# Performance work log

Measured on AMD Instinct MI355X. Metric: run time of the kernel, lower is better.

The kernel has to match this reference:

```python
import jax, jax.numpy as jnp
import numpy as np

B, L, D, H = 32, 128, 300, 1024
VOCAB = 32000


def setup_inputs() -> dict:
    key = jax.random.key(0)
    ks = jax.random.split(key, 8)
    sentence_embedding = jax.random.normal(ks[0], (B, L, D), dtype=jnp.float32)
    sentence_word = jax.random.randint(ks[1], (B, L), 0, VOCAB, dtype=jnp.int32)
    length = jax.random.randint(ks[2], (B,), L // 2, L + 1, dtype=jnp.int32)
    # leaf LSTMCell params (torch layout: weight [4H, in], gate order i,f,g,o)
    W_ih = jax.random.normal(ks[3], (4 * H, D), dtype=jnp.float32) * (2.0 / D) ** 0.5
    W_hh = jax.random.normal(ks[4], (4 * H, H), dtype=jnp.float32) * (1.0 / H) ** 0.5
    b_ih = jnp.zeros((4 * H,), jnp.float32).at[H:2 * H].set(1.0)  # forget bias = 1
    b_hh = jnp.zeros((4 * H,), jnp.float32)
    # NaryLSTMLayer: cat[h_l, h_x, h_r] (3H) -> gates i, f_l, f_x, f_r, u, o (6H)
    W_comp = jax.random.normal(ks[5], (6 * H, 3 * H), dtype=jnp.float32) * (2.0 / (3 * H)) ** 0.5
    b_comp = jnp.zeros((6 * H,), jnp.float32)
    return dict(sentence_embedding=sentence_embedding, W_ih=W_ih, W_hh=W_hh,
                b_ih=b_ih, b_hh=b_hh, W_comp=W_comp, b_comp=b_comp,
                sentence_word=sentence_word, length=length)


def _leaf_lstm(x, W_ih, W_hh, b_ih, b_hh):
    # x: (B, L, D) -> hs, cs: (B, L, H); vectorized over batch, scan over time
    h = W_hh.shape[1]
    h0 = jnp.zeros((x.shape[0], h), x.dtype)

    def step(carry, x_t):
        hp, cp = carry
        gates = x_t @ W_ih.T + b_ih + hp @ W_hh.T + b_hh
        i, f, g, o = jnp.split(gates, 4, axis=-1)
        c = jax.nn.sigmoid(f) * cp + jax.nn.sigmoid(i) * jnp.tanh(g)
        hn = jax.nn.sigmoid(o) * jnp.tanh(c)
        return (hn, c), (hn, c)

    _, (hs, cs) = jax.lax.scan(step, (h0, h0), jnp.swapaxes(x, 0, 1))
    return jnp.swapaxes(hs, 0, 1), jnp.swapaxes(cs, 0, 1)


def _compose(l, r, x, W_comp, b_comp):
    hl, cl = l
    hr, cr = r
    hx, cx = x
    a = jnp.concatenate([hl, hx, hr], axis=-1) @ W_comp.T + b_comp
    i, fl, fx, fr, u, o = jnp.split(a, 6, axis=-1)
    c = (jax.nn.sigmoid(i) * jnp.tanh(u) + jax.nn.sigmoid(fl) * cl
         + jax.nn.sigmoid(fx) * cx + jax.nn.sigmoid(fr) * cr)
    return jax.nn.sigmoid(o) * jnp.tanh(c), c


def _greedy_build(hs_i, cs_i, sc, start, end, zero, W_comp, b_comp):
    # sc: concrete numpy scores -> tree structure is a trace-time constant
    if end == start:
        return None
    if end == start + 1:
        return (hs_i[start], cs_i[start])
    pos = start + int(np.argmax(sc[start:end]))
    l = _greedy_build(hs_i, cs_i, sc, start, pos, zero, W_comp, b_comp)
    r = _greedy_build(hs_i, cs_i, sc, pos + 1, end, zero, W_comp, b_comp)
    if l is None:
        l = (zero, zero)
    if r is None:
        r = (zero, zero)
    return _compose(l, r, (hs_i[pos], cs_i[pos]), W_comp, b_comp)


def reference(sentence_embedding, W_ih, W_hh, b_ih, b_hh, W_comp, b_comp,
              sentence_word, length):
    hdim = W_hh.shape[1]
    hs, cs = _leaf_lstm(sentence_embedding, W_ih, W_hh, b_ih, b_hh)
    words = np.asarray(sentence_word)
    lens = np.asarray(length)
    # calc_score: 1 / (1 + df); vocab.id_to_df emulated as (w % 1000) + 1
    scores = 1.0 / (2.0 + (words % 1000).astype(np.float64))
    zero = jnp.zeros((hdim,), sentence_embedding.dtype)
    h_res, c_res = [], []
    for b in range(words.shape[0]):
        state = _greedy_build(hs[b], cs[b], scores[b], 0, int(lens[b]), zero,
                              W_comp, b_comp)
        h_res.append(state[0])
        c_res.append(state[1])
    return jnp.stack(h_res, axis=0), jnp.stack(c_res, axis=0)
```

## Files before the change

### kernel.cpp

```cpp
#include <hip/hip_runtime.h>

typedef unsigned short u16;
typedef __attribute__((ext_vector_type(8))) short short8;
typedef __attribute__((ext_vector_type(4))) float floatx4;

#define B_   32
#define L_   128
#define D_   300
#define DP_  320
#define H_   1024
#define G4_  4096
#define K3_  3072
#define NROUNDS 40

#define MO_MAXLEV 0
#define MO_ROOT   8
#define MO_LSTART 64
#define MO_LCOUNT 256
#define MO_FLG    448
#define MO_NODES  512
#define MO_CNT    4608
#define SPIN_CAP  500000
#define SPIN_CAP2 200000

#define FGRID 256
#define FTHREADS 512

#define MFMA(a,b,c) __builtin_amdgcn_mfma_f32_16x16x32_bf16((a),(b),(c),0,0,0)

__device__ inline float b2f(u16 u){ union { unsigned int i; float f; } v; v.i = ((unsigned int)u) << 16; return v.f; }
__device__ inline u16 f2b(float f){ union { float f; unsigned int i; } v; v.f = f; unsigned int r = v.i + 0x7FFFu + ((v.i >> 16) & 1u); return (u16)(r >> 16); }
__device__ inline float h2f(u16 u){ union { _Float16 h; u16 s; } v; v.s = u; return (float)v.h; }
__device__ inline u16 f2h(float f){ union { _Float16 h; u16 s; } v; v.h = (_Float16)f; return v.s; }
__device__ inline float sigf(float x){ return 1.f / (1.f + __expf(-x)); }
__device__ inline float tanh_(float x){ return 1.f - 2.f / (__expf(2.f * x) + 1.f); }
__device__ inline short8 cvt8(const float* p){
  floatx4 a = *(const floatx4*)p, b = *(const floatx4*)(p + 4);
  short8 r;
  r[0]=(short)f2b(a[0]); r[1]=(short)f2b(a[1]); r[2]=(short)f2b(a[2]); r[3]=(short)f2b(a[3]);
  r[4]=(short)f2b(b[0]); r[5]=(short)f2b(b[1]); r[6]=(short)f2b(b[2]); r[7]=(short)f2b(b[3]);
  return r;
}

__global__ void k_init(const float* __restrict__ emb, const float* __restrict__ Wih,
                       const float* __restrict__ Wcomp,
                       u16* __restrict__ embP, u16* __restrict__ WihP,
                       u16* __restrict__ WcompB,
                       u16* __restrict__ nodeH, float* __restrict__ nodeC, int* meta)
{
  const int gtid = blockIdx.x * 256 + threadIdx.x;
  const int nT = 2048 * 256;
  if (gtid < 64) meta[MO_FLG + gtid] = 0;
  for (int i = gtid; i < B_ * H_; i += nT) {
    int b = i >> 10, c = i & (H_ - 1);
    nodeH[(size_t)(b * 129 + 128) * H_ + c] = 0;
    nodeC[(size_t)(b * 129 + 128) * H_ + c] = 0.f;
  }
  for (int i = gtid; i < B_ * L_ * DP_; i += nT) {
    int r = i / DP_, k = i - r * DP_;
    embP[i] = (k < D_) ? f2b(emb[(size_t)r * D_ + k]) : (u16)0;
  }
  for (int i = gtid; i < G4_ * DP_; i += nT) {
    int r = i / DP_, k = i - r * DP_;
    WihP[i] = (k < D_) ? f2b(Wih[(size_t)r * D_ + k]) : (u16)0;
  }
  if (WcompB) {
    for (int c = gtid; c < (6 * H_ * K3_) / 8; c += nT)
      *(short8*)(WcompB + (size_t)c * 8) = cvt8(Wcomp + (size_t)c * 8);
  }
}

__global__ __launch_bounds__(256) void k_xg(const u16* __restrict__ embP,
    const u16* __restrict__ WihP, const float* __restrict__ bih,
    const float* __restrict__ bhh, u16* __restrict__ Xg)
{
  const int lane = threadIdx.x & 63, wave = threadIdx.x >> 6;
  const int l15 = lane & 15, quad = lane >> 4;
  const int gw = blockIdx.x * 4 + wave;
  for (int st = gw; st < 128 * 128; st += 2048 * 4) {
    int tm = st >> 7, tn = st & 127;
    int m0 = tm * 32, n0 = tn * 32;
    floatx4 acc[2][2] = {};
    for (int kc = 0; kc < DP_ / 32; ++kc) {
      int ko = kc * 32 + quad * 8;
      short8 a0 = *(const short8*)(embP + (size_t)(m0 + l15) * DP_ + ko);
      short8 a1 = *(const short8*)(embP + (size_t)(m0 + 16 + l15) * DP_ + ko);
      short8 b0 = *(const short8*)(WihP + (size_t)(n0 + l15) * DP_ + ko);
      short8 b1 = *(const short8*)(WihP + (size_t)(n0 + 16 + l15) * DP_ + ko);
      acc[0][0] = MFMA(a0, b0, acc[0][0]);
      acc[0][1] = MFMA(a0, b1, acc[0][1]);
      acc[1][0] = MFMA(a1, b0, acc[1][0]);
      acc[1][1] = MFMA(a1, b1, acc[1][1]);
    }
    for (int mi = 0; mi < 2; ++mi)
      for (int ni = 0; ni < 2; ++ni)
        for (int r = 0; r < 4; ++r) {
          int m = m0 + mi * 16 + quad * 4 + r;
          int n = n0 + ni * 16 + l15;
          float v = acc[mi][ni][r] + bih[n] + bhh[n];
          Xg[(size_t)m * G4_ + n] = f2h(v);
        }
  }
}

#define SCAN_LDS (65536 + 4*32*17*4)
__global__ __launch_bounds__(256, 1) void k_scan(const float* __restrict__ Whh,
    const u16* __restrict__ Xg, u16* __restrict__ nodeH,
    float* __restrict__ nodeC, u16* __restrict__ hEx, int* meta)
{
  extern __shared__ char smem[];
  u16*   hst = (u16*)smem;
  float* sG  = (float*)(smem + 65536);
  const int tid = threadIdx.x;
  const int g = tid >> 6, lane = tid & 63;
  const int l15 = lane & 15, quad = lane >> 4;
  const int n16 = blockIdx.x;
  int* flags = meta + MO_FLG;

  short8 bf[32];
#pragma unroll
  for (int kc = 0; kc < 32; ++kc)
    bf[kc] = cvt8(Whh + ((size_t)(g * 1024 + n16 * 16 + l15)) * 1024 + kc * 32 + quad * 8);

  const int cb = g * 8 + (lane & 7);
  const int cp = lane >> 3;
  const int c0 = n16 * 16 + cp * 2;

  float cst0 = 0.f, cst1 = 0.f;
  for (int t = 0; t < L_; ++t) {
    float xv[4][2];
    {
      const u16* xr = Xg + (size_t)(cb * 128 + t) * G4_;
#pragma unroll
      for (int gg = 0; gg < 4; ++gg)
#pragma unroll
        for (int u = 0; u < 2; ++u)
          xv[gg][u] = h2f(xr[gg * 1024 + c0 + u]);
    }
    floatx4 acc[2] = {};
    if (t > 0) {
      const unsigned long long* src =
          (const unsigned long long*)(hEx + ((t - 1) & 1) * (B_ * H_));
#pragma unroll
      for (int ch = 0; ch < 2; ++ch) {
        unsigned long long tmp[16];
#pragma unroll
        for (int q = 0; q < 16; ++q)
          tmp[q] = __hip_atomic_load(src + (ch * 16 + q) * 256 + tid,
                                     __ATOMIC_RELAXED, __HIP_MEMORY_SCOPE_AGENT);
#pragma unroll
        for (int q = 0; q < 16; ++q) {
          int idx = (ch * 16 + q) * 256 + tid;
          int b = idx >> 8, g8 = idx & 255, gr = g8 >> 1;
          *(unsigned long long*)(hst + (b << 10) + ((gr ^ (b & 7)) << 3) + (g8 & 1) * 4) = tmp[q];
        }
      }
      __syncthreads();
#pragma unroll
      for (int kc = 0; kc < 32; ++kc) {
        int gr = (kc * 4 + quad) ^ (l15 & 7);
        short8 a0 = *(const short8*)(hst + (l15 << 10) + (gr << 3));
        short8 a1 = *(const short8*)(hst + ((16 + l15) << 10) + (gr << 3));
        acc[0] = MFMA(a0, bf[kc], acc[0]);
        acc[1] = MFMA(a1, bf[kc], acc[1]);
      }
    }
#pragma unroll
    for (int mt = 0; mt < 2; ++mt)
#pragma unroll
      for (int r = 0; r < 4; ++r)
        sG[(g * 32 + mt * 16 + quad * 4 + r) * 17 + l15] = acc[mt][r];
    __syncthreads();
    {
      float cc[2] = { cst0, cst1 };
      float hh[2];
#pragma unroll
      for (int u = 0; u < 2; ++u) {
        int col = cp * 2 + u;
        float iv = sG[(0 * 32 + cb) * 17 + col] + xv[0][u];
        float fv = sG[(1 * 32 + cb) * 17 + col] + xv[1][u];
        float gv = sG[(2 * 32 + cb) * 17 + col] + xv[2][u];
        float ov = sG[(3 * 32 + cb) * 17 + col] + xv[3][u];
        float c = sigf(fv) * cc[u] + sigf(iv) * tanh_(gv);
        float h = sigf(ov) * tanh_(c);
        cc[u] = c; hh[u] = h;
      }
      cst0 = cc[0]; cst1 = cc[1];
      unsigned pack = (unsigned)f2b(hh[0]) | ((unsigned)f2b(hh[1]) << 16);
      __hip_atomic_store((unsigned*)(hEx + (t & 1) * (B_ * H_)) + (cb << 9) + (c0 >> 1),
                         pack, __ATOMIC_RELAXED, __HIP_MEMORY_SCOPE_AGENT);
      *(unsigned*)(nodeH + (size_t)(cb * 129 + t) * H_ + c0) = pack;
      *(float2*)(nodeC + (size_t)(cb * 129 + t) * H_ + c0) = make_float2(cc[0], cc[1]);
    }
    __syncthreads();
    if (tid == 0)
      __hip_atomic_store(&flags[n16], t + 1, __ATOMIC_RELAXED, __HIP_MEMORY_SCOPE_AGENT);
    if (g == 0) {
      int it = 0;
      for (;;) {
        int v = __hip_atomic_load(&flags[lane], __ATOMIC_RELAXED, __HIP_MEMORY_SCOPE_AGENT);
        if (__all(v >= t + 1) || ++it >= SPIN_CAP) break;
        __builtin_amdgcn_s_sleep(1);
      }
    }
    __syncthreads();
  }
}

__global__ void k_tree(const int* __restrict__ words, const int* __restrict__ lens,
                       int* meta)
{
  const int tid = threadIdx.x;
  __shared__ u16 sD[B_][L_];
  __shared__ short sL[B_][L_], sR[B_][L_];
  __shared__ short sS[B_][130];
  __shared__ short sO[B_][L_];
  __shared__ unsigned char sLev[B_][L_];
  __shared__ int sHist[132], sCur[132], sMaxLev;
  for (int i = tid; i < 132; i += 256) { sHist[i] = 0; sCur[i] = 0; }
  if (tid == 0) sMaxLev = 1;
  for (int i = tid; i < 256; i += 256) meta[MO_CNT + i] = 0;
  for (int i = tid; i < B_ * L_; i += 256) {
    int b = i >> 7, t = i & 127;
    sD[b][t] = (u16)(words[i] % 1000);
    sL[b][t] = -1; sR[b][t] = -1; sLev[b][t] = 0;
  }
  __syncthreads();
  if (tid < B_) {
    const int b = tid;
    int len = lens[b];
    if (len < 2) len = 2;
    if (len > 128) len = 128;
    int sp = 0;
    for (int i = 0; i < len; ++i) {
      int v = sD[b][i];
      int last = -1;
      while (sp > 0) {
        int top = sS[b][sp - 1];
        if ((int)sD[b][top] > v) { last = top; --sp; } else break;
      }
      sL[b][i] = (short)last;
      if (sp > 0) sR[b][sS[b][sp - 1]] = (short)i;
      sS[b][sp++] = (short)i;
    }
    const int root = sS[b][0];
    meta[MO_ROOT + b] = root;
    int cnt = 0, tp = 0;
    sS[b][tp++] = (short)root;
    while (tp > 0) {
      int p = sS[b][--tp];
      sO[b][cnt++] = (short)p;
      int l = sL[b][p], r = sR[b][p];
      if (l >= 0) sS[b][tp++] = (short)l;
      if (r >= 0) sS[b][tp++] = (short)r;
    }
    for (int k = cnt - 1; k >= 0; --k) {
      int p = sO[b][k];
      int l = sL[b][p], r = sR[b][p];
      if (l >= 0 || r >= 0) {
        int hl = (l >= 0) ? (int)sLev[b][l] : 0;
        int hr = (r >= 0) ? (int)sLev[b][r] : 0;
        sLev[b][p] = (unsigned char)(1 + (hl > hr ? hl : hr));
      }
    }
    atomicMax(&sMaxLev, (int)sLev[b][root]);
    for (int p = 0; p < len; ++p)
      if (sLev[b][p]) atomicAdd(&sHist[sLev[b][p]], 1);
  }
  __syncthreads();
  if (tid == 0) {
    int off2 = 0;
    for (int r = 1; r <= 128; ++r) {
      meta[MO_LSTART + r] = off2;
      sCur[r] = off2;
      meta[MO_LCOUNT + r] = sHist[r];
      off2 += sHist[r];
    }
    meta[MO_MAXLEV] = sMaxLev;
  }
  __syncthreads();
  if (tid < B_) {
    const int b = tid;
    int len = lens[b];
    if (len < 2) len = 2;
    if (len > 128) len = 128;
    for (int p = 0; p < len; ++p) if (sLev[b][p]) {
      int l = sL[b][p], r = sR[b][p];
      int le = (l < 0) ? 128 : (sLev[b][l] ? 129 + l : l);
      int re = (r < 0) ? 128 : (sLev[b][r] ? 129 + r : r);
      int idx = atomicAdd(&sCur[sLev[b][p]], 1);
      meta[MO_NODES + idx] = (b << 25) | (p << 18) | (le << 9) | re;
    }
  }
}

#define FOREST_LDS (147456 + 12288 + 512)
__global__ __launch_bounds__(FTHREADS, 2) void k_forest(const u16* __restrict__ Wc,
    const float* __restrict__ bcomp, const u16* __restrict__ nodeH,
    const float* __restrict__ nodeC, u16* __restrict__ compH,
    float* __restrict__ compC, int* meta)
{
  extern __shared__ char smem[];
  u16*   wlds  = (u16*)smem;
  float* sG    = (float*)(smem + 147456);
  int*   sInfo = (int*)(smem + 147456 + 12288);
  const int bcol = blockIdx.x;
  const int tid = threadIdx.x;
  const int w = tid >> 6, lane = tid & 63;
  const int l15 = lane & 15, quad = lane >> 4;
  int* flg = meta + MO_CNT;
  const int maxLev = meta[MO_MAXLEV];

  for (int j = tid; j < 9216; j += FTHREADS) {
    int idx = j / 24, r24 = j - idx * 24;
    int G = (r24 >> 2) * 1024 + bcol * 4 + (r24 & 3);
    *(short8*)(wlds + (size_t)j * 8) = *(const short8*)(Wc + (size_t)G * K3_ + idx * 8);
  }
  __syncthreads();

  for (int rd = 1; rd <= maxLev && rd <= 128; ++rd) {
    const int M = meta[MO_LCOUNT + rd];
    const int base = meta[MO_LSTART + rd];
    const int ntiles = (M + 127) >> 7;
    for (int tile = 0; tile < ntiles; ++tile) {
      __syncthreads();
      if (tid < 128) {
        int j = tile * 128 + tid; if (j >= M) j = M - 1;
        sInfo[tid] = meta[MO_NODES + base + j];
      }
      __syncthreads();
      {
        int info = sInfo[w * 16 + l15];
        int b = (info >> 25) & 31, p = (info >> 18) & 127;
        int li = (info >> 9) & 0x1FF, ri = info & 0x1FF;
        const u16* A0 = (li <= 128) ? nodeH + ((size_t)(b * 129 + li) << 10)
                                    : compH + ((size_t)(b * 128 + li - 129) << 10);
        const u16* A1 = nodeH + ((size_t)(b * 129 + p) << 10);
        const u16* A2 = (ri <= 128) ? nodeH + ((size_t)(b * 129 + ri) << 10)
                                    : compH + ((size_t)(b * 128 + ri - 129) << 10);
        const u16* Aseg[3] = { A0, A1, A2 };
        floatx4 acc0 = {}, acc1 = {};
#pragma unroll
        for (int seg = 0; seg < 3; ++seg) {
          const u16* Ap = Aseg[seg] + quad * 8;
          const u16* B0 = wlds + ((size_t)((seg * 128 + quad) * 24 + l15)) * 8;
          const u16* B1 = wlds + ((size_t)((seg * 128 + quad) * 24 + 16 + (l15 & 7))) * 8;
#pragma unroll 4
          for (int kcL = 0; kcL < 32; ++kcL) {
            short8 av = *(const short8*)(Ap + kcL * 32);
            acc0 = MFMA(av, *(const short8*)(B0 + kcL * 768), acc0);
            acc1 = MFMA(av, *(const short8*)(B1 + kcL * 768), acc1);
          }
        }
        float* sgw = sG + w * 384;
#pragma unroll
        for (int r = 0; r < 4; ++r)
          sgw[(quad * 4 + r) * 24 + l15] = acc0[r];
        if (l15 < 8)
#pragma unroll
          for (int r = 0; r < 4; ++r)
            sgw[(quad * 4 + r) * 24 + 16 + l15] = acc1[r];
      }
      __syncthreads();
      {
        int j_loc = tid >> 2, c = tid & 3;
        int j = tile * 128 + j_loc;
        if (j < M) {
          int info = sInfo[j_loc];
          int b = (info >> 25) & 31, p = (info >> 18) & 127;
          int li = (info >> 9) & 0x1FF, ri = info & 0x1FF;
          int hc = bcol * 4 + c;
          const float* gq = sG + (j_loc >> 4) * 384 + (j_loc & 15) * 24 + c;
          float gi  = gq[0]  + bcomp[hc];
          float gfl = gq[4]  + bcomp[H_ + hc];
          float gfx = gq[8]  + bcomp[2 * H_ + hc];
          float gfr = gq[12] + bcomp[3 * H_ + hc];
          float gu  = gq[16] + bcomp[4 * H_ + hc];
          float go  = gq[20] + bcomp[5 * H_ + hc];
          float cl  = (li <= 128) ? nodeC[(size_t)(b * 129 + li) * H_ + hc]
                                  : compC[(size_t)(b * 128 + li - 129) * H_ + hc];
          float cx  = nodeC[(size_t)(b * 129 + p) * H_ + hc];
          float cr2 = (ri <= 128) ? nodeC[(size_t)(b * 129 + ri) * H_ + hc]
                                  : compC[(size_t)(b * 128 + ri - 129) * H_ + hc];
          float cc = sigf(gi) * tanh_(gu) + sigf(gfl) * cl + sigf(gfx) * cx + sigf(gfr) * cr2;
          float hh = sigf(go) * tanh_(cc);
          __hip_atomic_store(&compH[(size_t)(b * 128 + p) * H_ + hc], f2b(hh),
                             __ATOMIC_RELAXED, __HIP_MEMORY_SCOPE_AGENT);
          compC[(size_t)(b * 128 + p) * H_ + hc] = cc;
        }
      }
    }
    __syncthreads();
    if (tid == 0)
      __hip_atomic_store(&flg[bcol], rd, __ATOMIC_RELAXED, __HIP_MEMORY_SCOPE_AGENT);
    if (w == 0) {
      int it = 0;
      for (;;) {
        int f0 = __hip_atomic_load(&flg[lane],       __ATOMIC_RELAXED, __HIP_MEMORY_SCOPE_AGENT);
        int f1 = __hip_atomic_load(&flg[lane + 64],  __ATOMIC_RELAXED, __HIP_MEMORY_SCOPE_AGENT);
        int f2 = __hip_atomic_load(&flg[lane + 128], __ATOMIC_RELAXED, __HIP_MEMORY_SCOPE_AGENT);
        int f3 = __hip_atomic_load(&flg[lane + 192], __ATOMIC_RELAXED, __HIP_MEMORY_SCOPE_AGENT);
        bool ok = (f0 >= rd) && (f1 >= rd) && (f2 >= rd) && (f3 >= rd);
        if (__all(ok) || ++it >= SPIN_CAP2) break;
        __builtin_amdgcn_s_sleep(1);
      }
    }
    __syncthreads();
  }
}

template<int BF16B>
__global__ __launch_bounds__(384) void k_round(const void* __restrict__ Wc,
    const float* __restrict__ bcomp, const u16* __restrict__ nodeH,
    const float* __restrict__ nodeC, u16* __restrict__ compH,
    float* __restrict__ compC, const int* __restrict__ meta, int rd)
{
  const int M = meta[MO_LCOUNT + rd];
  if (M <= 0 || M > 2048) return;
  const int mb = blockIdx.x >> 6, hs = blockIdx.x & 63;
  if (mb * 64 >= M) return;
  const int base = meta[MO_LSTART + rd];
  const int tid = threadIdx.x;
  const int w = tid >> 6, lane = tid & 63;
  const int l15 = lane & 15, quad = lane >> 4;
  __shared__ float sG[6][64][17];
  __shared__ int sInfo[64];
  if (tid < 64) {
    int j = mb * 64 + tid; if (j >= M) j = M - 1;
    sInfo[tid] = meta[MO_NODES + base + j];
  }
  __syncthreads();
  {
    const u16* aseg[3][4];
#pragma unroll
    for (int mi = 0; mi < 4; ++mi) {
      int info = sInfo[mi * 16 + l15];
      int b = (info >> 25) & 31, p = (info >> 18) & 127;
      int li = (info >> 9) & 0x1FF, ri = info & 0x1FF;
      aseg[0][mi] = (li <= 128) ? nodeH + ((size_t)(b * 129 + li) << 10)
                                : compH + ((size_t)(b * 128 + li - 129) << 10);
      aseg[1][mi] = nodeH + ((size_t)(b * 129 + p) << 10);
      aseg[2][mi] = (ri <= 128) ? nodeH + ((size_t)(b * 129 + ri) << 10)
                                : compH + ((size_t)(b * 128 + ri - 129) << 10);
    }
    floatx4 acc[4] = {};
    const size_t brow = (size_t)(w * 1024 + hs * 16 + l15) * K3_;
    for (int kc = 0; kc < 96; ++kc) {
      int seg = kc >> 5, ko = (kc & 31) * 32 + quad * 8;
      short8 bfr;
      if (BF16B) bfr = *(const short8*)((const u16*)Wc + brow + kc * 32 + quad * 8);
      else       bfr = cvt8((const float*)Wc + brow + kc * 32 + quad * 8);
      acc[0] = MFMA(*(const short8*)(aseg[seg][0] + ko), bfr, acc[0]);
      acc[1] = MFMA(*(const short8*)(aseg[seg][1] + ko), bfr, acc[1]);
      acc[2] = MFMA(*(const short8*)(aseg[seg][2] + ko), bfr, acc[2]);
      acc[3] = MFMA(*(const short8*)(aseg[seg][3] + ko), bfr, acc[3]);
    }
#pragma unroll
    for (int mi = 0; mi < 4; ++mi)
#pragma unroll
      for (int r = 0; r < 4; ++r) sG[w][mi * 16 + quad * 4 + r][l15] = acc[mi][r];
  }
  __syncthreads();
  for (int idx = tid; idx < 1024; idx += 384) {
    int j_loc = idx >> 4, col = idx & 15;
    int j = mb * 64 + j_loc;
    if (j < M) {
      int info = sInfo[j_loc];
      int b = (info >> 25) & 31, p = (info >> 18) & 127;
      int li = (info >> 9) & 0x1FF, ri = info & 0x1FF;
      int hc = hs * 16 + col;
      float gi  = sG[0][j_loc][col] + bcomp[hc];
      float gfl = sG[1][j_loc][col] + bcomp[H_ + hc];
      float gfx = sG[2][j_loc][col] + bcomp[2 * H_ + hc];
      float gfr = sG[3][j_loc][col] + bcomp[3 * H_ + hc];
      float gu  = sG[4][j_loc][col] + bcomp[4 * H_ + hc];
      float go  = sG[5][j_loc][col] + bcomp[5 * H_ + hc];
      float cl  = (li <= 128) ? nodeC[(size_t)(b * 129 + li) * H_ + hc]
                              : compC[(size_t)(b * 128 + li - 129) * H_ + hc];
      float cx  = nodeC[(size_t)(b * 129 + p) * H_ + hc];
      float cr2 = (ri <= 128) ? nodeC[(size_t)(b * 129 + ri) * H_ + hc]
                              : compC[(size_t)(b * 128 + ri - 129) * H_ + hc];
      float c = sigf(gi) * tanh_(gu) + sigf(gfl) * cl + sigf(gfx) * cx + sigf(gfr) * cr2;
      float h = sigf(go) * tanh_(c);
      compH[(size_t)(b * 128 + p) * H_ + hc] = f2b(h);
      compC[(size_t)(b * 128 + p) * H_ + hc] = c;
    }
  }
}

__global__ void k_out(const u16* __restrict__ compH, const float* __restrict__ compC,
                      const int* __restrict__ meta, float* __restrict__ out)
{
  int i = blockIdx.x * 256 + threadIdx.x;
  if (i >= 2 * B_ * H_) return;
  int part = i >> 15;
  int b = (i >> 10) & 31;
  int c = i & 1023;
  int root = meta[MO_ROOT + b] & 127;
  size_t rw = (size_t)(b * 128 + root) * H_ + c;
  out[i] = part ? compC[rw] : b2f(compH[rw]);
}

extern "C" void kernel_launch(void* const* d_in, const int* in_sizes, int n_in,
                              void* d_out, int out_size, void* d_ws, size_t ws_size,
                              hipStream_t stream)
{
  (void)in_sizes; (void)n_in; (void)out_size;
  const float* emb   = (const float*)d_in[0];
  const float* Wih   = (const float*)d_in[1];
  const float* Whh   = (const float*)d_in[2];
  const float* bih   = (const float*)d_in[3];
  const float* bhh   = (const float*)d_in[4];
  const float* Wcomp = (const float*)d_in[5];
  const float* bcomp = (const float*)d_in[6];
  const int* words   = (const int*)d_in[7];
  const int* lens    = (const int*)d_in[8];

  char* ws = (char*)d_ws;
  size_t off = 0;
  auto take = [&](size_t bytes) -> void* {
    void* p = ws + off; off += (bytes + 255) & ~(size_t)255; return p;
  };
  int*   meta  = (int*)  take((size_t)(512 + 4096 + 256) * 4);
  u16*   nodeH = (u16*)  take((size_t)B_ * 129 * H_ * 2);
  float* nodeC = (float*)take((size_t)B_ * 129 * H_ * 4);
  u16*   embP  = (u16*)  take((size_t)B_ * L_ * DP_ * 2);
  u16*   WihP  = (u16*)  take((size_t)G4_ * DP_ * 2);
  u16*   hEx   = (u16*)  take((size_t)2 * B_ * H_ * 2);
  char*  xgreg = (char*) take((size_t)B_ * L_ * G4_ * 2);
  u16*   Xg    = (u16*)  xgreg;
  u16*   compH = (u16*)  xgreg;
  float* compC = (float*)(xgreg + (size_t)B_ * 128 * H_ * 2);
  u16* WcompB = nullptr;
  if (off + (size_t)6 * H_ * K3_ * 2 <= ws_size)
    WcompB = (u16*)take((size_t)6 * H_ * K3_ * 2);

  hipFuncSetAttribute((const void*)k_scan,
                      hipFuncAttributeMaxDynamicSharedMemorySize, SCAN_LDS);
  hipFuncSetAttribute((const void*)k_forest,
                      hipFuncAttributeMaxDynamicSharedMemorySize, FOREST_LDS);

  k_init<<<dim3(2048), dim3(256), 0, stream>>>(emb, Wih, Wcomp, embP, WihP,
                                               WcompB, nodeH, nodeC, meta);
  k_xg  <<<dim3(2048), dim3(256), 0, stream>>>(embP, WihP, bih, bhh, Xg);
  k_scan<<<dim3(64), dim3(256), SCAN_LDS, stream>>>(Whh, Xg, nodeH, nodeC, hEx, meta);
  k_tree<<<dim3(1), dim3(256), 0, stream>>>(words, lens, meta);
  if (WcompB) {
    k_forest<<<dim3(FGRID), dim3(FTHREADS), FOREST_LDS, stream>>>(WcompB, bcomp,
                                                nodeH, nodeC, compH, compC, meta);
  } else {
    for (int rd = 1; rd <= NROUNDS; ++rd) {
      int maxM = 32 * 128 / (rd + 1);
      if (maxM > 2048) maxM = 2048;
      int nb = ((maxM + 63) / 64) * 64;
      k_round<0><<<dim3(nb), dim3(384), 0, stream>>>(Wcomp, bcomp, nodeH, nodeC,
                                                     compH, compC, meta, rd);
    }
  }
  k_out<<<dim3(256), dim3(256), 0, stream>>>(compH, compC, meta, (float*)d_out);
}
```

Before: 1.816 ms.

## Halve recurrent scan grid to 32 blocks of 512 threads with padded flags

The persistent LSTM scan kernel now runs 32 workgroups of 512 threads instead of 64 of 256, each block covering 32 hidden columns across two wave groups. Fewer blocks take part in the per-timestep grid-wide flag barrier and in the global broadcast of h. Flags are spread 16 ints apart to avoid false sharing, and each block starts its h reads at a different offset to spread memory traffic. The cost is more register and LDS use per block and fewer CUs doing the per-step matmul.

```diff
diff --git a/kernel.cpp b/kernel.cpp
--- a/kernel.cpp
+++ b/kernel.cpp
@@ -20,6 +20,7 @@
 #define MO_FLG    448
 #define MO_NODES  512
 #define MO_CNT    4608
+#define MO_SFLG   4864
 #define SPIN_CAP  500000
 #define SPIN_CAP2 200000
 
@@ -51,6 +52,7 @@
   const int gtid = blockIdx.x * 256 + threadIdx.x;
   const int nT = 2048 * 256;
   if (gtid < 64) meta[MO_FLG + gtid] = 0;
+  if (gtid < 512) meta[MO_SFLG + gtid] = 0;
   for (int i = gtid; i < B_ * H_; i += nT) {
     int b = i >> 10, c = i & (H_ - 1);
     nodeH[(size_t)(b * 129 + 128) * H_ + c] = 0;
@@ -103,8 +105,8 @@
   }
 }
 
-#define SCAN_LDS (65536 + 4*32*17*4)
-__global__ __launch_bounds__(256, 1) void k_scan(const float* __restrict__ Whh,
+#define SCAN_LDS (65536 + 128*36*4)
+__global__ __launch_bounds__(512, 1) void k_scan(const float* __restrict__ Whh,
     const u16* __restrict__ Xg, u16* __restrict__ nodeH,
     float* __restrict__ nodeC, u16* __restrict__ hEx, int* meta)
 {
@@ -112,19 +114,22 @@
   u16*   hst = (u16*)smem;
   float* sG  = (float*)(smem + 65536);
   const int tid = threadIdx.x;
-  const int g = tid >> 6, lane = tid & 63;
+  const int w = tid >> 6, lane = tid & 63;
+  const int g = w & 3, ch = w >> 2;
   const int l15 = lane & 15, quad = lane >> 4;
-  const int n16 = blockIdx.x;
-  int* flags = meta + MO_FLG;
+  const int n32 = blockIdx.x;
+  int* sflg = meta + MO_SFLG;
 
   short8 bf[32];
 #pragma unroll
   for (int kc = 0; kc < 32; ++kc)
-    bf[kc] = cvt8(Whh + ((size_t)(g * 1024 + n16 * 16 + l15)) * 1024 + kc * 32 + quad * 8);
-
-  const int cb = g * 8 + (lane & 7);
-  const int cp = lane >> 3;
-  const int c0 = n16 * 16 + cp * 2;
+    bf[kc] = cvt8(Whh + ((size_t)(g * 1024 + n32 * 32 + ch * 16 + l15)) * 1024
+                  + kc * 32 + quad * 8);
+
+  const int cb = tid >> 4;
+  const int cp = tid & 15;
+  const int c0loc = cp * 2;
+  const int c0 = n32 * 32 + c0loc;
 
   float cst0 = 0.f, cst1 = 0.f;
   for (int t = 0; t < L_; ++t) {
@@ -141,19 +146,19 @@
     if (t > 0) {
       const unsigned long long* src =
           (const unsigned long long*)(hEx + ((t - 1) & 1) * (B_ * H_));
-#pragma unroll
-      for (int ch = 0; ch < 2; ++ch) {
-        unsigned long long tmp[16];
-#pragma unroll
-        for (int q = 0; q < 16; ++q)
-          tmp[q] = __hip_atomic_load(src + (ch * 16 + q) * 256 + tid,
-                                     __ATOMIC_RELAXED, __HIP_MEMORY_SCOPE_AGENT);
-#pragma unroll
-        for (int q = 0; q < 16; ++q) {
-          int idx = (ch * 16 + q) * 256 + tid;
-          int b = idx >> 8, g8 = idx & 255, gr = g8 >> 1;
-          *(unsigned long long*)(hst + (b << 10) + ((gr ^ (b & 7)) << 3) + (g8 & 1) * 4) = tmp[q];
-        }
+      unsigned long long tmp[16];
+#pragma unroll
+      for (int q = 0; q < 16; ++q) {
+        int qq = (q + n32) & 15;
+        tmp[q] = __hip_atomic_load(src + qq * 512 + tid,
+                                   __ATOMIC_RELAXED, __HIP_MEMORY_SCOPE_AGENT);
+      }
+#pragma unroll
+      for (int q = 0; q < 16; ++q) {
+        int qq = (q + n32) & 15;
+        int idx = qq * 512 + tid;
+        int b = idx >> 8, g8 = idx & 255, gr = g8 >> 1;
+        *(unsigned long long*)(hst + (b << 10) + ((gr ^ (b & 7)) << 3) + (g8 & 1) * 4) = tmp[q];
       }
       __syncthreads();
 #pragma unroll
@@ -169,18 +174,18 @@
     for (int mt = 0; mt < 2; ++mt)
 #pragma unroll
       for (int r = 0; r < 4; ++r)
-        sG[(g * 32 + mt * 16 + quad * 4 + r) * 17 + l15] = acc[mt][r];
+        sG[(g * 32 + mt * 16 + quad * 4 + r) * 36 + ch * 16 + l15] = acc[mt][r];
     __syncthreads();
     {
       float cc[2] = { cst0, cst1 };
       float hh[2];
 #pragma unroll
       for (int u = 0; u < 2; ++u) {
-        int col = cp * 2 + u;
-        float iv = sG[(0 * 32 + cb) * 17 + col] + xv[0][u];
-        float fv = sG[(1 * 32 + cb) * 17 + col] + xv[1][u];
-        float gv = sG[(2 * 32 + cb) * 17 + col] + xv[2][u];
-        float ov = sG[(3 * 32 + cb) * 17 + col] + xv[3][u];
+        int col = c0loc + u;
+        float iv = sG[(0 * 32 + cb) * 36 + col] + xv[0][u];
+        float fv = sG[(1 * 32 + cb) * 36 + col] + xv[1][u];
+        float gv = sG[(2 * 32 + cb) * 36 + col] + xv[2][u];
+        float ov = sG[(3 * 32 + cb) * 36 + col] + xv[3][u];
         float c = sigf(fv) * cc[u] + sigf(iv) * tanh_(gv);
         float h = sigf(ov) * tanh_(c);
         cc[u] = c; hh[u] = h;
@@ -194,11 +199,13 @@
     }
     __syncthreads();
     if (tid == 0)
-      __hip_atomic_store(&flags[n16], t + 1, __ATOMIC_RELAXED, __HIP_MEMORY_SCOPE_AGENT);
-    if (g == 0) {
+      __hip_atomic_store(&sflg[n32 * 16], t + 1, __ATOMIC_RELAXED, __HIP_MEMORY_SCOPE_AGENT);
+    if (w == 0) {
       int it = 0;
       for (;;) {
-        int v = __hip_atomic_load(&flags[lane], __ATOMIC_RELAXED, __HIP_MEMORY_SCOPE_AGENT);
+        int v = (lane < 32)
+          ? __hip_atomic_load(&sflg[lane * 16], __ATOMIC_RELAXED, __HIP_MEMORY_SCOPE_AGENT)
+          : 0x7fffffff;
         if (__all(v >= t + 1) || ++it >= SPIN_CAP) break;
         __builtin_amdgcn_s_sleep(1);
       }
@@ -521,7 +528,7 @@
   auto take = [&](size_t bytes) -> void* {
     void* p = ws + off; off += (bytes + 255) & ~(size_t)255; return p;
   };
-  int*   meta  = (int*)  take((size_t)(512 + 4096 + 256) * 4);
+  int*   meta  = (int*)  take((size_t)(512 + 4096 + 256 + 512) * 4);
   u16*   nodeH = (u16*)  take((size_t)B_ * 129 * H_ * 2);
   float* nodeC = (float*)take((size_t)B_ * 129 * H_ * 4);
   u16*   embP  = (u16*)  take((size_t)B_ * L_ * DP_ * 2);
@@ -543,7 +550,7 @@
   k_init<<<dim3(2048), dim3(256), 0, stream>>>(emb, Wih, Wcomp, embP, WihP,
                                                WcompB, nodeH, nodeC, meta);
   k_xg  <<<dim3(2048), dim3(256), 0, stream>>>(embP, WihP, bih, bhh, Xg);
-  k_scan<<<dim3(64), dim3(256), SCAN_LDS, stream>>>(Whh, Xg, nodeH, nodeC, hEx, meta);
+  k_scan<<<dim3(32), dim3(512), SCAN_LDS, stream>>>(Whh, Xg, nodeH, nodeC, hEx, meta);
   k_tree<<<dim3(1), dim3(256), 0, stream>>>(words, lens, meta);
   if (WcompB) {
     k_forest<<<dim3(FGRID), dim3(FTHREADS), FOREST_LDS, stream>>>(WcompB, bcomp,
```

After: 1.712 ms. 5.7% less time.
